# Performance work log

Hardware: AMD Instinct MI355X
Metric: run time of the kernel (lower is better)

## Reference

```python
import jax, jax.numpy as jnp
import numpy as np

H = 16      # attention heads
D = 1024    # embedding size
HD = 64     # head size = D // H


def setup_inputs() -> dict:
    key = jax.random.key(0)
    ks = jax.random.split(key, 6)
    s = 1.0 / np.sqrt(D)
    x = jax.random.normal(ks[0], (2, 2048, D), dtype=jnp.float32)
    Wq = jax.random.normal(ks[1], (H, D, HD), dtype=jnp.float32) * s
    Wk = jax.random.normal(ks[2], (H, D, HD), dtype=jnp.float32) * s
    Wv = jax.random.normal(ks[3], (H, D, HD), dtype=jnp.float32) * s
    Wo = jax.random.normal(ks[4], (H * HD, D), dtype=jnp.float32) * s
    bo = jax.random.normal(ks[5], (D,), dtype=jnp.float32) * 0.01
    return {"x": x, "Wq": Wq, "Wk": Wk, "Wv": Wv, "Wo": Wo, "bo": bo}


def reference(x, Wq, Wk, Wv, Wo, bo):
    # x: [B, S, D]; per-head projections batched over the head axis.
    B, S, _ = x.shape
    q = jnp.einsum('bsd,hde->bhse', x, Wq)  # [B,H,S,HD]
    k = jnp.einsum('bsd,hde->bhse', x, Wk)
    v = jnp.einsum('bsd,hde->bhse', x, Wv)
    scale = 1.0 / jnp.sqrt(jnp.asarray(HD, dtype=x.dtype))
    scores = jnp.einsum('bhqe,bhke->bhqk', q, k) * scale  # [B,H,S,S]
    causal = jnp.tril(jnp.ones((S, S), dtype=bool))
    scores = jnp.where(causal, scores, jnp.asarray(-jnp.inf, dtype=x.dtype))
    attn = jax.nn.softmax(scores, axis=-1)
    out = jnp.einsum('bhqk,bhke->bhqe', attn, v)  # [B,H,S,HD]
    # concat heads along last dim (head order matches ModuleList order)
    out = out.transpose(0, 2, 1, 3).reshape(B, S, H * HD)
    return out @ Wo + bo  # dropout is identity in eval mode
```

## Files before the change

kernel.cpp:

```cpp
#include <hip/hip_runtime.h>
#include <hip/hip_bf16.h>
#include <cstdint>

#define Hh 16
#define Dd 1024
#define HD 64
#define Bb 2
#define Ss 2048

typedef float f32x4 __attribute__((ext_vector_type(4)));
typedef __bf16 bf16x8 __attribute__((ext_vector_type(8)));

__device__ __forceinline__ unsigned short f2bf(float f) {
  union { float f; unsigned u; } v; v.f = f;
  unsigned r = (v.u + 0x7FFFu + ((v.u >> 16) & 1u)) >> 16;
  return (unsigned short)r;
}

__device__ __forceinline__ void gld16(const void* g, void* l) {
  __builtin_amdgcn_global_load_lds(
      (__attribute__((address_space(1))) void*)(g),
      (__attribute__((address_space(3))) void*)(l),
      16, 0, 0);
}

__global__ __launch_bounds__(256)
void pack_x_k(const float4* __restrict__ x, unsigned short* __restrict__ xb, int n4) {
  const int i = blockIdx.x * blockDim.x + threadIdx.x;
  if (i >= n4) return;
  const float4 v = x[i];
  ushort4 o;
  o.x = f2bf(v.x); o.y = f2bf(v.y); o.z = f2bf(v.z); o.w = f2bf(v.w);
  *(ushort4*)&xb[(size_t)i * 4] = o;
}

__global__ __launch_bounds__(256)
void tconv_k(const float* __restrict__ in, unsigned short* __restrict__ out,
             int R, int C, float scale) {
  __shared__ float T[64][65];
  const int m = blockIdx.z;
  const float* src = in + (size_t)m * R * C;
  unsigned short* dst = out + (size_t)m * R * C;
  const int c0 = blockIdx.x * 64, r0 = blockIdx.y * 64;
  const int tx = threadIdx.x & 63, ty = threadIdx.x >> 6;
#pragma unroll
  for (int it = 0; it < 16; ++it) {
    const int i = ty + it * 4;
    T[i][tx] = src[(size_t)(r0 + i) * C + c0 + tx];
  }
  __syncthreads();
#pragma unroll
  for (int it = 0; it < 16; ++it) {
    const int jj = ty + it * 4;
    dst[(size_t)(c0 + jj) * R + r0 + tx] = f2bf(T[tx][jj] * scale);
  }
}

__global__ __launch_bounds__(256)
void gemm_qkv(const unsigned short* __restrict__ A,
              const unsigned short* __restrict__ Bt,
              unsigned short* __restrict__ q_out,
              unsigned short* __restrict__ k_out,
              unsigned short* __restrict__ vt_out)
{
  __shared__ unsigned short As[2][128 * 64];
  __shared__ unsigned short Bs[2][128 * 64];

  const int K = 1024;
  const int tid = threadIdx.x;
  const int w = tid >> 6, lane = tid & 63;
  const int lo = lane & 15, hi = lane >> 4;
  const int wr = w >> 1, wc = w & 1;
  const int row0 = blockIdx.y * 128;
  const int col0 = blockIdx.x * 128;
  const bool isv = (col0 >= 2048);

  f32x4 acc[4][4] = {};

  const int srow = w * 32 + (lane >> 3);
  const int scol = ((lane & 7) ^ (lane >> 3)) * 8;
  const int swl  = (lo & 7) << 4;

#define GSTAGE(bi, k0)                                                    \
  _Pragma("unroll")                                                       \
  for (int c = 0; c < 4; ++c) {                                           \
    const int rr = srow + c * 8;                                          \
    gld16(A  + (size_t)(row0 + rr) * K + ((k0) + scol),                   \
          (char*)&As[bi][0] + (w * 4 + c) * 1024);                        \
    gld16(Bt + (size_t)(col0 + rr) * K + ((k0) + scol),                   \
          (char*)&Bs[bi][0] + (w * 4 + c) * 1024);                        \
  }

  GSTAGE(0, 0);
  __syncthreads();

  int cur = 0;
  for (int t = 0; t < 16; ++t) {
    if (t + 1 < 16) { GSTAGE(cur ^ 1, (t + 1) * 64); }
#pragma unroll
    for (int ks = 0; ks < 2; ++ks) {
      bf16x8 af[4], bfr[4];
#pragma unroll
      for (int i = 0; i < 4; ++i)
        af[i] = *(const bf16x8*)((const char*)&As[cur][0] +
                 (wr * 64 + i * 16 + lo) * 128 + ((ks * 64 + hi * 16) ^ swl));
#pragma unroll
      for (int j = 0; j < 4; ++j)
        bfr[j] = *(const bf16x8*)((const char*)&Bs[cur][0] +
                 (wc * 64 + j * 16 + lo) * 128 + ((ks * 64 + hi * 16) ^ swl));
      __builtin_amdgcn_s_setprio(1);
      if (isv) {
#pragma unroll
        for (int i = 0; i < 4; ++i)
#pragma unroll
          for (int j = 0; j < 4; ++j)
            acc[i][j] = __builtin_amdgcn_mfma_f32_16x16x32_bf16(af[i], bfr[j], acc[i][j], 0, 0, 0);
      } else {
#pragma unroll
        for (int i = 0; i < 4; ++i)
#pragma unroll
          for (int j = 0; j < 4; ++j)
            acc[i][j] = __builtin_amdgcn_mfma_f32_16x16x32_bf16(bfr[j], af[i], acc[i][j], 0, 0, 0);
      }
      __builtin_amdgcn_s_setprio(0);
    }
    __syncthreads();
    cur ^= 1;
  }

#pragma unroll
  for (int i = 0; i < 4; ++i) {
#pragma unroll
    for (int j = 0; j < 4; ++j) {
      if (isv) {
        const int grow = row0 + wr * 64 + i * 16 + hi * 4;
        const int gcol = col0 + wc * 64 + j * 16 + lo;
        const int hd = (gcol >> 6) & 15, e = gcol & 63;
        const int bb2 = grow >> 11, s = grow & 2047;
        ushort4 pk;
        pk.x = f2bf(acc[i][j][0]); pk.y = f2bf(acc[i][j][1]);
        pk.z = f2bf(acc[i][j][2]); pk.w = f2bf(acc[i][j][3]);
        *(ushort4*)&vt_out[((size_t)(bb2 * Hh + hd) * HD + e) * Ss + s] = pk;
      } else {
        const int m  = row0 + wr * 64 + i * 16 + lo;
        const int n0 = col0 + wc * 64 + j * 16 + hi * 4;
        const int p = n0 >> 10;
        const int hd = (n0 >> 6) & 15, e = n0 & 63;
        const int bb2 = m >> 11, s = m & 2047;
        unsigned short* dst = (p == 0) ? q_out : k_out;
        ushort4 pk;
        pk.x = f2bf(acc[i][j][0]); pk.y = f2bf(acc[i][j][1]);
        pk.z = f2bf(acc[i][j][2]); pk.w = f2bf(acc[i][j][3]);
        *(ushort4*)&dst[((size_t)(bb2 * Hh + hd) * Ss + s) * HD + e] = pk;
      }
    }
  }
#undef GSTAGE
}

__global__ __launch_bounds__(256)
void gemm_out(const unsigned short* __restrict__ A,
              const unsigned short* __restrict__ Bt,
              float* __restrict__ o_out,
              const float* __restrict__ bias)
{
  __shared__ unsigned short As[2][128 * 64];
  __shared__ unsigned short Bs[2][128 * 64];

  const int K = 1024, Ndim = 1024;
  const int tid = threadIdx.x;
  const int w = tid >> 6, lane = tid & 63;
  const int lo = lane & 15, hi = lane >> 4;
  const int wr = w >> 1, wc = w & 1;
  const int row0 = blockIdx.y * 128;
  const int col0 = blockIdx.x * 128;

  f32x4 acc[4][4] = {};

  const int srow = w * 32 + (lane >> 3);
  const int scol = ((lane & 7) ^ (lane >> 3)) * 8;
  const int swl  = (lo & 7) << 4;

#define GSTAGE(bi, k0)                                                    \
  _Pragma("unroll")                                                       \
  for (int c = 0; c < 4; ++c) {                                           \
    const int rr = srow + c * 8;                                          \
    gld16(A  + (size_t)(row0 + rr) * K + ((k0) + scol),                   \
          (char*)&As[bi][0] + (w * 4 + c) * 1024);                        \
    gld16(Bt + (size_t)(col0 + rr) * K + ((k0) + scol),                   \
          (char*)&Bs[bi][0] + (w * 4 + c) * 1024);                        \
  }

  GSTAGE(0, 0);
  __syncthreads();

  int cur = 0;
  for (int t = 0; t < 16; ++t) {
    if (t + 1 < 16) { GSTAGE(cur ^ 1, (t + 1) * 64); }
#pragma unroll
    for (int ks = 0; ks < 2; ++ks) {
      bf16x8 af[4], bfr[4];
#pragma unroll
      for (int i = 0; i < 4; ++i)
        af[i] = *(const bf16x8*)((const char*)&As[cur][0] +
                 (wr * 64 + i * 16 + lo) * 128 + ((ks * 64 + hi * 16) ^ swl));
#pragma unroll
      for (int j = 0; j < 4; ++j)
        bfr[j] = *(const bf16x8*)((const char*)&Bs[cur][0] +
                 (wc * 64 + j * 16 + lo) * 128 + ((ks * 64 + hi * 16) ^ swl));
      __builtin_amdgcn_s_setprio(1);
#pragma unroll
      for (int i = 0; i < 4; ++i)
#pragma unroll
        for (int j = 0; j < 4; ++j)
          acc[i][j] = __builtin_amdgcn_mfma_f32_16x16x32_bf16(bfr[j], af[i], acc[i][j], 0, 0, 0);
      __builtin_amdgcn_s_setprio(0);
    }
    __syncthreads();
    cur ^= 1;
  }

#pragma unroll
  for (int i = 0; i < 4; ++i) {
#pragma unroll
    for (int j = 0; j < 4; ++j) {
      const int m  = row0 + wr * 64 + i * 16 + lo;
      const int n0 = col0 + wc * 64 + j * 16 + hi * 4;
      const float4 bv = *(const float4*)&bias[n0];
      float4 o;
      o.x = acc[i][j][0] + bv.x; o.y = acc[i][j][1] + bv.y;
      o.z = acc[i][j][2] + bv.z; o.w = acc[i][j][3] + bv.w;
      *(float4*)&o_out[(size_t)m * Ndim + n0] = o;
    }
  }
#undef GSTAGE
}

__global__ __launch_bounds__(256)
void attn_fwd(const unsigned short* __restrict__ qb,
              const unsigned short* __restrict__ kb,
              const unsigned short* __restrict__ vtb,
              unsigned short* __restrict__ ob)
{
  __shared__ unsigned short Ks[2][64 * 64];
  __shared__ unsigned short Vs[2][64 * 64];

  const int qt = 31 - blockIdx.y;
  const int bh = blockIdx.x;
  const int bb2 = bh >> 4;
  const int hd = bh & 15;

  const unsigned short* Q  = qb  + (size_t)bh * Ss * HD;
  const unsigned short* Kg = kb  + (size_t)bh * Ss * HD;
  const unsigned short* Vt = vtb + (size_t)bh * HD * Ss;

  const int tid = threadIdx.x;
  const int w = tid >> 6, lane = tid & 63;
  const int lo = lane & 15, hi = lane >> 4;
  const int qrow0 = qt * 64 + w * 16;

  const int sr   = lane >> 3;
  const int scol = ((lane & 7) ^ sr) * 8;
  int prow[2];
#pragma unroll
  for (int c = 0; c < 2; ++c) {
    const int L = c * 4 + w;
    prow[c] = (L >> 2) * 32 + ((L & 1) * 2 + (sr >> 2)) * 8 + ((L >> 1) & 1) * 4 + (sr & 3);
  }

#define STAGE(bi, kv)                                                     \
  _Pragma("unroll")                                                       \
  for (int c = 0; c < 2; ++c) {                                           \
    const int L = c * 4 + w;                                              \
    gld16(Kg + (size_t)((kv) + prow[c]) * HD + scol,                      \
          (char*)&Ks[bi][0] + L * 1024);                                  \
    gld16(Vt + (size_t)(L * 8 + sr) * Ss + (kv) + scol,                   \
          (char*)&Vs[bi][0] + L * 1024);                                  \
  }

  const int swl = (lo & 7) << 4;

  bf16x8 vones;
#pragma unroll
  for (int j = 0; j < 8; ++j) vones[j] = (__bf16)1.0f;

  bf16x8 qf[2];
#pragma unroll
  for (int ks = 0; ks < 2; ++ks)
    qf[ks] = *(const bf16x8*)&Q[(size_t)(qrow0 + lo) * HD + ks * 32 + hi * 8];

  f32x4 oacc[4] = {};
  float m2s = -INFINITY;
  float l2[4];
#pragma unroll
  for (int r = 0; r < 4; ++r) l2[r] = 0.f;

  const int ntiles = qt + 1;

  STAGE(0, 0);
  __syncthreads();

  int cur = 0;
  for (int t = 0; t < ntiles; ++t) {
    if (t + 1 < ntiles) { STAGE(cur ^ 1, (t + 1) * 64); }

    f32x4 sacc[4] = {};
    __builtin_amdgcn_s_setprio(1);
#pragma unroll
    for (int ks = 0; ks < 2; ++ks) {
      bf16x8 kf[4];
#pragma unroll
      for (int nj = 0; nj < 4; ++nj)
        kf[nj] = *(const bf16x8*)((const char*)&Ks[cur][0] +
                 (nj * 16 + lo) * 128 + ((ks * 64 + hi * 16) ^ swl));
#pragma unroll
      for (int nj = 0; nj < 4; ++nj)
        sacc[nj] = __builtin_amdgcn_mfma_f32_16x16x32_bf16(kf[nj], qf[ks], sacc[nj], 0, 0, 0);
    }
    __builtin_amdgcn_s_setprio(0);

    if (t == qt) {
      const int qr = w * 16 + lo;
#pragma unroll
      for (int nj = 0; nj < 4; ++nj) {
        const int kb0 = (nj >> 1) * 32 + (nj & 1) * 4 + hi * 8;
#pragma unroll
        for (int r = 0; r < 4; ++r)
          if (kb0 + r > qr) sacc[nj][r] = -INFINITY;
      }
    }

    float a0 = fmaxf(fmaxf(sacc[0][0], sacc[0][1]), fmaxf(sacc[0][2], sacc[0][3]));
    float a1 = fmaxf(fmaxf(sacc[1][0], sacc[1][1]), fmaxf(sacc[1][2], sacc[1][3]));
    float a2 = fmaxf(fmaxf(sacc[2][0], sacc[2][1]), fmaxf(sacc[2][2], sacc[2][3]));
    float a3 = fmaxf(fmaxf(sacc[3][0], sacc[3][1]), fmaxf(sacc[3][2], sacc[3][3]));
    const float lmax = fmaxf(fmaxf(a0, a1), fmaxf(a2, a3));
    if (!__all(lmax - m2s <= 8.0f)) {
      float rm = lmax;
      rm = fmaxf(rm, __shfl_xor(rm, 16, 64));
      rm = fmaxf(rm, __shfl_xor(rm, 32, 64));
      const float mn = fmaxf(m2s, rm);
      const float rcs = __builtin_amdgcn_exp2f(m2s - mn);
      m2s = mn;
#pragma unroll
      for (int r = 0; r < 4; ++r) {
        const float rc = __shfl(rcs, hi * 4 + r, 64);
        l2[r] *= rc;
#pragma unroll
        for (int nj = 0; nj < 4; ++nj)
          oacc[nj][r] *= rc;
      }
    }

    bf16x8 pa[2];
#pragma unroll
    for (int ks = 0; ks < 2; ++ks)
#pragma unroll
      for (int j = 0; j < 4; ++j) {
        pa[ks][j]     = (__bf16)__builtin_amdgcn_exp2f(sacc[2 * ks][j]     - m2s);
        pa[ks][4 + j] = (__bf16)__builtin_amdgcn_exp2f(sacc[2 * ks + 1][j] - m2s);
      }

    f32x4 osum = {};
    __builtin_amdgcn_s_setprio(1);
#pragma unroll
    for (int ks = 0; ks < 2; ++ks) {
      bf16x8 vf[4];
#pragma unroll
      for (int nj = 0; nj < 4; ++nj)
        vf[nj] = *(const bf16x8*)((const char*)&Vs[cur][0] +
                 (nj * 16 + lo) * 128 + ((ks * 64 + hi * 16) ^ swl));
#pragma unroll
      for (int nj = 0; nj < 4; ++nj)
        oacc[nj] = __builtin_amdgcn_mfma_f32_16x16x32_bf16(pa[ks], vf[nj], oacc[nj], 0, 0, 0);
      osum = __builtin_amdgcn_mfma_f32_16x16x32_bf16(pa[ks], vones, osum, 0, 0, 0);
    }
    __builtin_amdgcn_s_setprio(0);
#pragma unroll
    for (int r = 0; r < 4; ++r)
      l2[r] += osum[r];

    __syncthreads();
    cur ^= 1;
  }
#undef STAGE

#pragma unroll
  for (int r = 0; r < 4; ++r) {
    const int s = qrow0 + hi * 4 + r;
    const float il = 1.0f / l2[r];
    const size_t base = ((size_t)bb2 * Ss + s) * Dd + hd * HD;
#pragma unroll
    for (int nj = 0; nj < 4; ++nj)
      ob[base + nj * 16 + lo] = f2bf(oacc[nj][r] * il);
  }
}

extern "C" void kernel_launch(void* const* d_in, const int* in_sizes, int n_in,
                              void* d_out, int out_size, void* d_ws, size_t ws_size,
                              hipStream_t stream)
{
  const float* x  = (const float*)d_in[0];
  const float* Wq = (const float*)d_in[1];
  const float* Wk = (const float*)d_in[2];
  const float* Wv = (const float*)d_in[3];
  const float* Wo = (const float*)d_in[4];
  const float* bo = (const float*)d_in[5];
  float* out = (float*)d_out;

  char* ws = (char*)d_ws;
  unsigned short* xb    = (unsigned short*)(ws);
  unsigned short* wqkvT = (unsigned short*)(ws + 8388608);
  unsigned short* woT   = (unsigned short*)(ws + 14680064);
  unsigned short* qb    = (unsigned short*)(ws + 16777216);
  unsigned short* kb    = (unsigned short*)(ws + 25165824);
  unsigned short* vtb   = (unsigned short*)(ws + 33554432);
  unsigned short* ob    = (unsigned short*)(ws + 41943040);

  pack_x_k<<<4096, 256, 0, stream>>>((const float4*)x, xb, 1048576);
  tconv_k<<<dim3(1, 16, 16), 256, 0, stream>>>(Wq, wqkvT,           1024, 64, 0.18033688011112042f);
  tconv_k<<<dim3(1, 16, 16), 256, 0, stream>>>(Wk, wqkvT + 1048576, 1024, 64, 1.0f);
  tconv_k<<<dim3(1, 16, 16), 256, 0, stream>>>(Wv, wqkvT + 2097152, 1024, 64, 1.0f);
  tconv_k<<<dim3(16, 16, 1), 256, 0, stream>>>(Wo, woT,             1024, 1024, 1.0f);

  gemm_qkv<<<dim3(24, 32), 256, 0, stream>>>(xb, wqkvT, qb, kb, vtb);
  attn_fwd<<<dim3(32, 32), 256, 0, stream>>>(qb, kb, vtb, ob);
  gemm_out<<<dim3(8, 32), 256, 0, stream>>>(ob, woT, out, bo);
}
```

Measured before the change: 131.8 us.

## Merge QKV weight conversions, drop GEMM double-buffering, halve output GEMM row tile

```diff
diff --git a/kernel.cpp b/kernel.cpp
--- a/kernel.cpp
+++ b/kernel.cpp
@@ -35,24 +35,46 @@
 }
 
 __global__ __launch_bounds__(256)
-void tconv_k(const float* __restrict__ in, unsigned short* __restrict__ out,
-             int R, int C, float scale) {
+void tconv_qkv(const float* __restrict__ Wq, const float* __restrict__ Wk,
+               const float* __restrict__ Wv, unsigned short* __restrict__ out,
+               float qscale) {
   __shared__ float T[64][65];
   const int m = blockIdx.z;
-  const float* src = in + (size_t)m * R * C;
-  unsigned short* dst = out + (size_t)m * R * C;
+  const float* base = (m < 16) ? Wq : (m < 32) ? Wk : Wv;
+  const float scale = (m < 16) ? qscale : 1.0f;
+  const float* src = base + (size_t)(m & 15) * 1024 * 64;
+  unsigned short* dst = out + (size_t)m * 1024 * 64;
+  const int r0 = blockIdx.y * 64;
+  const int tx = threadIdx.x & 63, ty = threadIdx.x >> 6;
+#pragma unroll
+  for (int it = 0; it < 16; ++it) {
+    const int i = ty + it * 4;
+    T[i][tx] = src[(size_t)(r0 + i) * 64 + tx];
+  }
+  __syncthreads();
+#pragma unroll
+  for (int it = 0; it < 16; ++it) {
+    const int jj = ty + it * 4;
+    dst[(size_t)jj * 1024 + r0 + tx] = f2bf(T[tx][jj] * scale);
+  }
+}
+
+__global__ __launch_bounds__(256)
+void tconv_k(const float* __restrict__ in, unsigned short* __restrict__ out,
+             int R, int C) {
+  __shared__ float T[64][65];
   const int c0 = blockIdx.x * 64, r0 = blockIdx.y * 64;
   const int tx = threadIdx.x & 63, ty = threadIdx.x >> 6;
 #pragma unroll
   for (int it = 0; it < 16; ++it) {
     const int i = ty + it * 4;
-    T[i][tx] = src[(size_t)(r0 + i) * C + c0 + tx];
+    T[i][tx] = in[(size_t)(r0 + i) * C + c0 + tx];
   }
   __syncthreads();
 #pragma unroll
   for (int it = 0; it < 16; ++it) {
     const int jj = ty + it * 4;
-    dst[(size_t)(c0 + jj) * R + r0 + tx] = f2bf(T[tx][jj] * scale);
+    out[(size_t)(c0 + jj) * R + r0 + tx] = f2bf(T[tx][jj]);
   }
 }
 
@@ -63,8 +85,8 @@
               unsigned short* __restrict__ k_out,
               unsigned short* __restrict__ vt_out)
 {
-  __shared__ unsigned short As[2][128 * 64];
-  __shared__ unsigned short Bs[2][128 * 64];
+  __shared__ unsigned short As[128 * 64];
+  __shared__ unsigned short Bs[128 * 64];
 
   const int K = 1024;
   const int tid = threadIdx.x;
@@ -81,32 +103,27 @@
   const int scol = ((lane & 7) ^ (lane >> 3)) * 8;
   const int swl  = (lo & 7) << 4;
 
-#define GSTAGE(bi, k0)                                                    \
-  _Pragma("unroll")                                                       \
-  for (int c = 0; c < 4; ++c) {                                           \
-    const int rr = srow + c * 8;                                          \
-    gld16(A  + (size_t)(row0 + rr) * K + ((k0) + scol),                   \
-          (char*)&As[bi][0] + (w * 4 + c) * 1024);                        \
-    gld16(Bt + (size_t)(col0 + rr) * K + ((k0) + scol),                   \
-          (char*)&Bs[bi][0] + (w * 4 + c) * 1024);                        \
-  }
-
-  GSTAGE(0, 0);
-  __syncthreads();
-
-  int cur = 0;
   for (int t = 0; t < 16; ++t) {
-    if (t + 1 < 16) { GSTAGE(cur ^ 1, (t + 1) * 64); }
+    const int k0 = t * 64;
+#pragma unroll
+    for (int c = 0; c < 4; ++c) {
+      const int rr = srow + c * 8;
+      gld16(A  + (size_t)(row0 + rr) * K + (k0 + scol),
+            (char*)As + (w * 4 + c) * 1024);
+      gld16(Bt + (size_t)(col0 + rr) * K + (k0 + scol),
+            (char*)Bs + (w * 4 + c) * 1024);
+    }
+    __syncthreads();
 #pragma unroll
     for (int ks = 0; ks < 2; ++ks) {
       bf16x8 af[4], bfr[4];
 #pragma unroll
       for (int i = 0; i < 4; ++i)
-        af[i] = *(const bf16x8*)((const char*)&As[cur][0] +
+        af[i] = *(const bf16x8*)((const char*)As +
                  (wr * 64 + i * 16 + lo) * 128 + ((ks * 64 + hi * 16) ^ swl));
 #pragma unroll
       for (int j = 0; j < 4; ++j)
-        bfr[j] = *(const bf16x8*)((const char*)&Bs[cur][0] +
+        bfr[j] = *(const bf16x8*)((const char*)Bs +
                  (wc * 64 + j * 16 + lo) * 128 + ((ks * 64 + hi * 16) ^ swl));
       __builtin_amdgcn_s_setprio(1);
       if (isv) {
@@ -125,7 +142,6 @@
       __builtin_amdgcn_s_setprio(0);
     }
     __syncthreads();
-    cur ^= 1;
   }
 
 #pragma unroll
@@ -155,7 +171,6 @@
       }
     }
   }
-#undef GSTAGE
 }
 
 __global__ __launch_bounds__(256)
@@ -164,67 +179,61 @@
               float* __restrict__ o_out,
               const float* __restrict__ bias)
 {
-  __shared__ unsigned short As[2][128 * 64];
-  __shared__ unsigned short Bs[2][128 * 64];
+  __shared__ unsigned short As[64 * 64];
+  __shared__ unsigned short Bs[128 * 64];
 
   const int K = 1024, Ndim = 1024;
   const int tid = threadIdx.x;
   const int w = tid >> 6, lane = tid & 63;
   const int lo = lane & 15, hi = lane >> 4;
   const int wr = w >> 1, wc = w & 1;
-  const int row0 = blockIdx.y * 128;
+  const int row0 = blockIdx.y * 64;
   const int col0 = blockIdx.x * 128;
 
-  f32x4 acc[4][4] = {};
-
-  const int srow = w * 32 + (lane >> 3);
-  const int scol = ((lane & 7) ^ (lane >> 3)) * 8;
+  f32x4 acc[2][4] = {};
+
+  const int sr   = lane >> 3;
+  const int scol = ((lane & 7) ^ sr) * 8;
   const int swl  = (lo & 7) << 4;
 
-#define GSTAGE(bi, k0)                                                    \
-  _Pragma("unroll")                                                       \
-  for (int c = 0; c < 4; ++c) {                                           \
-    const int rr = srow + c * 8;                                          \
-    gld16(A  + (size_t)(row0 + rr) * K + ((k0) + scol),                   \
-          (char*)&As[bi][0] + (w * 4 + c) * 1024);                        \
-    gld16(Bt + (size_t)(col0 + rr) * K + ((k0) + scol),                   \
-          (char*)&Bs[bi][0] + (w * 4 + c) * 1024);                        \
-  }
-
-  GSTAGE(0, 0);
-  __syncthreads();
-
-  int cur = 0;
   for (int t = 0; t < 16; ++t) {
-    if (t + 1 < 16) { GSTAGE(cur ^ 1, (t + 1) * 64); }
+    const int k0 = t * 64;
+#pragma unroll
+    for (int c = 0; c < 2; ++c)
+      gld16(A + (size_t)(row0 + c * 32 + w * 8 + sr) * K + (k0 + scol),
+            (char*)As + c * 4096 + w * 1024);
+#pragma unroll
+    for (int c = 0; c < 4; ++c)
+      gld16(Bt + (size_t)(col0 + c * 32 + w * 8 + sr) * K + (k0 + scol),
+            (char*)Bs + c * 4096 + w * 1024);
+    __syncthreads();
 #pragma unroll
     for (int ks = 0; ks < 2; ++ks) {
-      bf16x8 af[4], bfr[4];
-#pragma unroll
-      for (int i = 0; i < 4; ++i)
-        af[i] = *(const bf16x8*)((const char*)&As[cur][0] +
-                 (wr * 64 + i * 16 + lo) * 128 + ((ks * 64 + hi * 16) ^ swl));
+      bf16x8 af[2], bfr[4];
+#pragma unroll
+      for (int i = 0; i < 2; ++i)
+        af[i] = *(const bf16x8*)((const char*)As +
+                 (wr * 32 + i * 16 + lo) * 128 + ((ks * 64 + hi * 16) ^ swl));
 #pragma unroll
       for (int j = 0; j < 4; ++j)
-        bfr[j] = *(const bf16x8*)((const char*)&Bs[cur][0] +
+        bfr[j] = *(const bf16x8*)((const char*)Bs +
                  (wc * 64 + j * 16 + lo) * 128 + ((ks * 64 + hi * 16) ^ swl));
       __builtin_amdgcn_s_setprio(1);
 #pragma unroll
-      for (int i = 0; i < 4; ++i)
+      for (int i = 0; i < 2; ++i)
 #pragma unroll
         for (int j = 0; j < 4; ++j)
           acc[i][j] = __builtin_amdgcn_mfma_f32_16x16x32_bf16(bfr[j], af[i], acc[i][j], 0, 0, 0);
       __builtin_amdgcn_s_setprio(0);
     }
     __syncthreads();
-    cur ^= 1;
-  }
-
-#pragma unroll
-  for (int i = 0; i < 4; ++i) {
+  }
+
+#pragma unroll
+  for (int i = 0; i < 2; ++i) {
 #pragma unroll
     for (int j = 0; j < 4; ++j) {
-      const int m  = row0 + wr * 64 + i * 16 + lo;
+      const int m  = row0 + wr * 32 + i * 16 + lo;
       const int n0 = col0 + wc * 64 + j * 16 + hi * 4;
       const float4 bv = *(const float4*)&bias[n0];
       float4 o;
@@ -233,7 +242,6 @@
       *(float4*)&o_out[(size_t)m * Ndim + n0] = o;
     }
   }
-#undef GSTAGE
 }
 
 __global__ __launch_bounds__(256)
@@ -418,12 +426,11 @@
   unsigned short* ob    = (unsigned short*)(ws + 41943040);
 
   pack_x_k<<<4096, 256, 0, stream>>>((const float4*)x, xb, 1048576);
-  tconv_k<<<dim3(1, 16, 16), 256, 0, stream>>>(Wq, wqkvT,           1024, 64, 0.18033688011112042f);
-  tconv_k<<<dim3(1, 16, 16), 256, 0, stream>>>(Wk, wqkvT + 1048576, 1024, 64, 1.0f);
-  tconv_k<<<dim3(1, 16, 16), 256, 0, stream>>>(Wv, wqkvT + 2097152, 1024, 64, 1.0f);
-  tconv_k<<<dim3(16, 16, 1), 256, 0, stream>>>(Wo, woT,             1024, 1024, 1.0f);
+  tconv_qkv<<<dim3(1, 16, 48), 256, 0, stream>>>(Wq, Wk, Wv, wqkvT,
+                                                 0.18033688011112042f);
+  tconv_k<<<dim3(16, 16, 1), 256, 0, stream>>>(Wo, woT, 1024, 1024);
 
   gemm_qkv<<<dim3(24, 32), 256, 0, stream>>>(xb, wqkvT, qb, kb, vtb);
   attn_fwd<<<dim3(32, 32), 256, 0, stream>>>(qb, kb, vtb, ob);
-  gemm_out<<<dim3(8, 32), 256, 0, stream>>>(ob, woT, out, bo);
-}
+  gemm_out<<<dim3(8, 64), 256, 0, stream>>>(ob, woT, out, bo);
+}
```

New measurement: 124.4 us. -5.6%, faster.
